# Kernel optimization log

Hardware: AMD Instinct MI355X
Metric: run time of the kernel (lower is better)

Reference implementation:

```python
import jax, jax.numpy as jnp
import numpy as np

B, S, D = 8, 2048, 1024      # batch, seq (tokens), in/out token dim
E = 2 * D                    # expansion dim (expansion_factor=2)
SDIM = 128                   # attention feature dim s
SQRT_S = float(np.sqrt(SDIM))
EPS_LN = 1e-5                # ScaleNorm eps


def setup_inputs() -> dict:
    key = jax.random.key(0)
    ks = jax.random.split(key, 8)
    return {
        "x": jax.random.normal(ks[0], (B, S, D), jnp.float32),
        "pos_enc": jax.random.normal(ks[1], (S, SDIM), jnp.float32),
        "ln_g": jnp.ones((1,), jnp.float32),                                   # ScaleNorm scalar gain
        "uv_w": jax.random.normal(ks[2], (2 * E + SDIM, D), jnp.float32) / np.sqrt(D),  # fused uv proj (xavier-ish)
        "gamma": jax.random.uniform(ks[3], (2, SDIM), jnp.float32),            # q/k affine scale
        "beta": jax.random.uniform(ks[4], (2, SDIM), jnp.float32),             # q/k affine shift
        "o_w": jax.random.normal(ks[5], (D, E), jnp.float32) / np.sqrt(E),     # output proj
        "res_scale": jnp.ones((D,), jnp.float32),                              # ChannelWiseScale
    }


def reference(x, pos_enc, ln_g, uv_w, gamma, beta, o_w, res_scale):
    # ScaleNorm: x / clamp(||x|| * d^-0.5, eps) * g
    norm = jnp.linalg.norm(x, axis=-1, keepdims=True) * (D ** -0.5)
    xn = x / jnp.maximum(norm, EPS_LN) * ln_g
    # fused uv projection + SiLU
    uv = jax.nn.silu(xn @ uv_w.T)                      # [B,S,2E+s]
    u = uv[..., :E]                                    # gate
    v = uv[..., E:2 * E]                               # values
    base = uv[..., 2 * E:]                             # shared q/k base [B,S,s]
    qk_base = base[..., None, :] * gamma + beta        # [B,S,2,s]
    q = qk_base[..., 0, :] + pos_enc                   # add positional enc [B,S,s]
    k = qk_base[..., 1, :] + pos_enc
    # squared-ReLU attention kernel
    kernel = jnp.square(jax.nn.relu(jnp.einsum('bqs,bks->bqk', q, k) / SQRT_S))
    out = (u * jnp.einsum('bqk,bke->bqe', kernel, v)) @ o_w.T  # [B,S,D]
    # channel-wise scaled residual (in_dims == out_dims -> shortcut)
    return x * res_scale + out
```

## Files before the change

### kernel.cpp

```cpp
#include <hip/hip_runtime.h>
#include <stdint.h>

#define B_   8
#define S_   2048
#define D_   1024
#define E_   2048
#define SD_  128
#define M_   (B_ * S_)
#define NUV  (2 * E_ + SD_)

typedef __attribute__((ext_vector_type(8))) short short8;
typedef __attribute__((ext_vector_type(4))) float floatx4;

__device__ __forceinline__ ushort f2bf(float f) {
    uint32_t u = __float_as_uint(f);
    uint32_t r = (u + 0x7fffu + ((u >> 16) & 1u)) >> 16;
    return (ushort)r;
}
__device__ __forceinline__ float bf2f(ushort h) {
    return __uint_as_float(((uint32_t)h) << 16);
}
__device__ __forceinline__ float silu(float z) {
    return z * __builtin_amdgcn_rcpf(1.0f + __expf(-z));
}

__device__ __forceinline__ void tile_swizzle(int& mt, int& nt) {
    const int gx  = gridDim.x;
    const int lin = blockIdx.y * gx + blockIdx.x;
    const int band = lin / (gx * 8);
    const int r    = lin - band * gx * 8;
    mt = band * 8 + (r & 7);
    nt = r >> 3;
}

__device__ __forceinline__ void gemm_core(
    const ushort* __restrict__ A, const ushort* __restrict__ B,
    int lda, int ldb, int K, int m0, int n0,
    ushort* ldsA, ushort* ldsB, floatx4 acc[4][4])
{
    const int t    = threadIdx.x;
    const int lane = t & 63;
    const int l15  = lane & 15;
    const int quad = lane >> 4;
    const int wave = t >> 6;
    const int wm   = (wave >> 1) * 64;
    const int wn   = (wave & 1) * 64;
    const int key  = l15 & 7;

    const ushort* gA[4]; const ushort* gB[4];
    ushort* lA[4]; ushort* lB[4];
    #pragma unroll
    for (int i = 0; i < 4; ++i) {
        const int c   = t + i * 256;
        const int row = c >> 3;
        const int gkc = ((c & 7) ^ (row & 7)) * 8;
        gA[i] = A + (size_t)(m0 + row) * lda + gkc;
        gB[i] = B + (size_t)(n0 + row) * ldb + gkc;
        lA[i] = ldsA + c * 8;
        lB[i] = ldsB + c * 8;
    }

    short8 rA[4], rB[4];
    #pragma unroll
    for (int i = 0; i < 4; ++i) rA[i] = *(const short8*)gA[i];
    #pragma unroll
    for (int i = 0; i < 4; ++i) rB[i] = *(const short8*)gB[i];

    for (int kk = 0; kk < K; kk += 64) {
        __syncthreads();
        #pragma unroll
        for (int i = 0; i < 4; ++i) *(short8*)lA[i] = rA[i];
        #pragma unroll
        for (int i = 0; i < 4; ++i) *(short8*)lB[i] = rB[i];
        __syncthreads();

        if (kk + 64 < K) {
            #pragma unroll
            for (int i = 0; i < 4; ++i) rA[i] = *(const short8*)(gA[i] + kk + 64);
            #pragma unroll
            for (int i = 0; i < 4; ++i) rB[i] = *(const short8*)(gB[i] + kk + 64);
        }

        #pragma unroll
        for (int s = 0; s < 2; ++s) {
            const int koff = ((s * 4 + quad) ^ key) * 8;
            short8 af[4], bfr[4];
            #pragma unroll
            for (int mi = 0; mi < 4; ++mi)
                af[mi] = *(const short8*)(ldsA + (wm + mi * 16 + l15) * 64 + koff);
            #pragma unroll
            for (int ni = 0; ni < 4; ++ni)
                bfr[ni] = *(const short8*)(ldsB + (wn + ni * 16 + l15) * 64 + koff);
            #pragma unroll
            for (int mi = 0; mi < 4; ++mi)
                #pragma unroll
                for (int ni = 0; ni < 4; ++ni)
                    acc[mi][ni] = __builtin_amdgcn_mfma_f32_16x16x32_bf16(
                        af[mi], bfr[ni], acc[mi][ni], 0, 0, 0);
        }
    }
}

#define EPI_INDICES \
    const int t = threadIdx.x; \
    const int lane = t & 63, l15 = lane & 15, quad = lane >> 4; \
    const int wave = t >> 6, wm = (wave >> 1) * 64, wn = (wave & 1) * 64; \
    (void)t;

#define ZERO_ACC \
    floatx4 acc[4][4]; \
    _Pragma("unroll") \
    for (int i = 0; i < 4; ++i) \
        _Pragma("unroll") \
        for (int j = 0; j < 4; ++j) \
            _Pragma("unroll") \
            for (int r = 0; r < 4; ++r) acc[i][j][r] = 0.0f;

__global__ __launch_bounds__(256) void k_cvt(const float* __restrict__ src,
                                             ushort* __restrict__ dst, int n4) {
    int i = blockIdx.x * 256 + threadIdx.x;
    if (i < n4) {
        float4 v = ((const float4*)src)[i];
        ushort4 o;
        o.x = f2bf(v.x); o.y = f2bf(v.y); o.z = f2bf(v.z); o.w = f2bf(v.w);
        ((ushort4*)dst)[i] = o;
    }
}

__global__ __launch_bounds__(256) void k_rmsnorm(const float* __restrict__ x,
                                                 const float* __restrict__ ln_g,
                                                 ushort* __restrict__ xnb) {
    const int m = blockIdx.x;
    const int t = threadIdx.x;
    float4 v = ((const float4*)(x + (size_t)m * D_))[t];
    float ss = v.x * v.x + v.y * v.y + v.z * v.z + v.w * v.w;
    #pragma unroll
    for (int off = 32; off > 0; off >>= 1) ss += __shfl_down(ss, off, 64);
    __shared__ float red[4];
    if ((t & 63) == 0) red[t >> 6] = ss;
    __syncthreads();
    float tot = red[0] + red[1] + red[2] + red[3];
    float rms = sqrtf(tot * (1.0f / (float)D_));
    float scale = ln_g[0] / fmaxf(rms, 1e-5f);
    ushort4 o;
    o.x = f2bf(v.x * scale); o.y = f2bf(v.y * scale);
    o.z = f2bf(v.z * scale); o.w = f2bf(v.w * scale);
    ((ushort4*)(xnb + (size_t)m * D_))[t] = o;
}

__global__ __launch_bounds__(256) void k_gemm1(
    const ushort* __restrict__ xnb, const ushort* __restrict__ uvwb,
    const float* __restrict__ gamma, const float* __restrict__ beta,
    const float* __restrict__ pos,
    ushort* __restrict__ u, ushort* __restrict__ vT,
    ushort* __restrict__ qb, ushort* __restrict__ kb)
{
    __shared__ __align__(16) ushort lds[17408];
    ushort* ldsA = lds;
    ushort* ldsB = lds + 8192;
    ZERO_ACC
    int mt, nt;
    tile_swizzle(mt, nt);
    const int m0 = mt * 128;
    const int n0 = nt * 128;
    gemm_core(xnb, uvwb, D_, D_, D_, m0, n0, ldsA, ldsB, acc);
    EPI_INDICES

    if (nt < 16) {
        #pragma unroll
        for (int mi = 0; mi < 4; ++mi)
            #pragma unroll
            for (int ni = 0; ni < 4; ++ni) {
                const int col = n0 + wn + ni * 16 + l15;
                #pragma unroll
                for (int r = 0; r < 4; ++r) {
                    const int row = m0 + wm + mi * 16 + quad * 4 + r;
                    u[(size_t)row * E_ + col] = f2bf(silu(acc[mi][ni][r]));
                }
            }
    } else if (nt < 32) {
        const int b   = m0 >> 11;
        const int s0  = m0 & (S_ - 1);
        const int ec0 = n0 - E_;
        __syncthreads();
        #pragma unroll
        for (int mi = 0; mi < 4; ++mi)
            #pragma unroll
            for (int ni = 0; ni < 4; ++ni) {
                const int col = wn + ni * 16 + l15;
                const int row = wm + mi * 16 + quad * 4;
                #pragma unroll
                for (int r = 0; r < 4; r += 2) {
                    ushort2 pr;
                    pr.x = f2bf(silu(acc[mi][ni][r]));
                    pr.y = f2bf(silu(acc[mi][ni][r + 1]));
                    *(ushort2*)&lds[col * 136 + row + r] = pr;
                }
            }
        __syncthreads();
        ushort* vTb = vT + ((size_t)b * E_ + ec0) * S_ + s0;
        #pragma unroll
        for (int i = 0; i < 8; ++i) {
            const int lin = i * 256 + t;
            const int e  = lin >> 4;
            const int sb = (lin & 15) * 8;
            *(short8*)(vTb + (size_t)e * S_ + sb) = *(const short8*)&lds[e * 136 + sb];
        }
    } else {
        #pragma unroll
        for (int mi = 0; mi < 4; ++mi)
            #pragma unroll
            for (int ni = 0; ni < 4; ++ni) {
                const int sd = wn + ni * 16 + l15;
                const float g0 = gamma[sd], g1 = gamma[SD_ + sd];
                const float be0 = beta[sd], be1 = beta[SD_ + sd];
                #pragma unroll
                for (int r = 0; r < 4; ++r) {
                    const int row = m0 + wm + mi * 16 + quad * 4 + r;
                    const int srow = row & (S_ - 1);
                    float s = silu(acc[mi][ni][r]);
                    const float p = pos[(size_t)srow * SD_ + sd];
                    qb[(size_t)row * SD_ + sd] = f2bf(s * g0 + be0 + p);
                    kb[(size_t)row * SD_ + sd] = f2bf(s * g1 + be1 + p);
                }
            }
    }
}

__global__ __launch_bounds__(256) void k_scores(
    const ushort* __restrict__ qb, const ushort* __restrict__ kb,
    ushort* __restrict__ kern, int b_off)
{
    __shared__ __align__(16) ushort ldsA[128 * 64];
    __shared__ __align__(16) ushort ldsB[128 * 64];
    ZERO_ACC
    const int bz = blockIdx.z;
    const int b  = b_off + bz;
    int mt, nt;
    tile_swizzle(mt, nt);
    const int m0 = mt * 128;
    const int n0 = nt * 128;
    gemm_core(qb + (size_t)b * S_ * SD_, kb + (size_t)b * S_ * SD_,
              SD_, SD_, SD_, m0, n0, ldsA, ldsB, acc);
    EPI_INDICES
    ushort* ko = kern + (size_t)bz * S_ * S_;
    const float inv = 0.08838834764831845f;
    #pragma unroll
    for (int mi = 0; mi < 4; ++mi)
        #pragma unroll
        for (int ni = 0; ni < 4; ++ni) {
            const int col = n0 + wn + ni * 16 + l15;
            #pragma unroll
            for (int r = 0; r < 4; ++r) {
                const int row = m0 + wm + mi * 16 + quad * 4 + r;
                float s = fmaxf(acc[mi][ni][r] * inv, 0.0f);
                ko[(size_t)row * S_ + col] = f2bf(s * s);
            }
        }
}

__global__ __launch_bounds__(256) void k_kv(
    const ushort* __restrict__ kern, const ushort* __restrict__ vT,
    const ushort* __restrict__ u, ushort* __restrict__ kvu, int b_off)
{
    __shared__ __align__(16) ushort ldsA[128 * 64];
    __shared__ __align__(16) ushort ldsB[128 * 64];
    ZERO_ACC
    const int bz = blockIdx.z;
    const int b  = b_off + bz;
    int mt, nt;
    tile_swizzle(mt, nt);
    const int m0 = mt * 128;
    const int n0 = nt * 128;
    gemm_core(kern + (size_t)bz * S_ * S_, vT + (size_t)b * E_ * S_,
              S_, S_, S_, m0, n0, ldsA, ldsB, acc);
    EPI_INDICES
    #pragma unroll
    for (int mi = 0; mi < 4; ++mi)
        #pragma unroll
        for (int ni = 0; ni < 4; ++ni) {
            const int col = n0 + wn + ni * 16 + l15;
            #pragma unroll
            for (int r = 0; r < 4; ++r) {
                const int row = m0 + wm + mi * 16 + quad * 4 + r;
                const size_t gi = (size_t)(b * S_ + row) * E_ + col;
                float uval = bf2f(u[gi]);
                kvu[gi] = f2bf(uval * acc[mi][ni][r]);
            }
        }
}

__global__ __launch_bounds__(256) void k_out(
    const ushort* __restrict__ kvu, const ushort* __restrict__ owb,
    const float* __restrict__ x, const float* __restrict__ res_scale,
    float* __restrict__ out)
{
    __shared__ __align__(16) ushort ldsA[128 * 64];
    __shared__ __align__(16) ushort ldsB[128 * 64];
    ZERO_ACC
    int mt, nt;
    tile_swizzle(mt, nt);
    const int m0 = mt * 128;
    const int n0 = nt * 128;
    gemm_core(kvu, owb, E_, E_, E_, m0, n0, ldsA, ldsB, acc);
    EPI_INDICES
    #pragma unroll
    for (int mi = 0; mi < 4; ++mi)
        #pragma unroll
        for (int ni = 0; ni < 4; ++ni) {
            const int col = n0 + wn + ni * 16 + l15;
            const float rs = res_scale[col];
            #pragma unroll
            for (int r = 0; r < 4; ++r) {
                const int row = m0 + wm + mi * 16 + quad * 4 + r;
                const size_t gi = (size_t)row * D_ + col;
                out[gi] = x[gi] * rs + acc[mi][ni][r];
            }
        }
}

extern "C" void kernel_launch(void* const* d_in, const int* in_sizes, int n_in,
                              void* d_out, int out_size, void* d_ws, size_t ws_size,
                              hipStream_t stream)
{
    const float* x         = (const float*)d_in[0];
    const float* pos       = (const float*)d_in[1];
    const float* ln_g      = (const float*)d_in[2];
    const float* uv_w      = (const float*)d_in[3];
    const float* gamma     = (const float*)d_in[4];
    const float* beta      = (const float*)d_in[5];
    const float* o_w       = (const float*)d_in[6];
    const float* res_scale = (const float*)d_in[7];
    float* out = (float*)d_out;

    char* p = (char*)d_ws;
    ushort* region0 = (ushort*)p; p += (size_t)M_ * D_ * 2;
    ushort* uvwb    = (ushort*)p; p += (size_t)NUV * D_ * 2;
    ushort* owb     = (ushort*)p; p += (size_t)D_ * E_ * 2;
    ushort* u       = (ushort*)p; p += (size_t)M_ * E_ * 2;
    ushort* kvu     = (ushort*)p; p += (size_t)M_ * E_ * 2;
    ushort* vT      = (ushort*)p; p += (size_t)M_ * E_ * 2;
    ushort* qb      = (ushort*)p; p += (size_t)M_ * SD_ * 2;
    ushort* kb      = (ushort*)p; p += (size_t)M_ * SD_ * 2;

    ushort* xnb  = region0;
    ushort* kern = region0;

    k_cvt<<<(NUV * D_ / 4 + 255) / 256, 256, 0, stream>>>(uv_w, uvwb, NUV * D_ / 4);
    k_cvt<<<(D_ * E_ / 4 + 255) / 256, 256, 0, stream>>>(o_w, owb, D_ * E_ / 4);
    k_rmsnorm<<<M_, 256, 0, stream>>>(x, ln_g, xnb);
    k_gemm1<<<dim3(NUV / 128, M_ / 128), 256, 0, stream>>>(xnb, uvwb, gamma, beta, pos, u, vT, qb, kb);
    for (int g = 0; g < 2; ++g) {
        k_scores<<<dim3(S_ / 128, S_ / 128, 4), 256, 0, stream>>>(qb, kb, kern, g * 4);
        k_kv<<<dim3(E_ / 128, S_ / 128, 4), 256, 0, stream>>>(kern, vT, u, kvu, g * 4);
    }
    k_out<<<dim3(D_ / 128, M_ / 128), 256, 0, stream>>>(kvu, owb, x, res_scale, out);
}
```

Baseline: 648.5 us.

## Use direct global-to-LDS loads, finer tile swizzle, and raise occupancy bound

Replaces the register-staged global-to-LDS copy with global_load_lds DMA loads directly into shared memory. This drops the register prefetch, which frees VGPRs, and adds a min-blocks-per-CU of 3 to launch bounds on all GEMM kernels so more workgroups can be resident. Tile swizzle now groups N tiles in chunks of 4 within each 8-row band to improve L2 reuse. The cost is losing the software prefetch overlap: the loads are now issued and waited on between the two barriers, with no double buffering, so each K step may stall on memory latency.

```diff
diff --git a/kernel.cpp b/kernel.cpp
--- a/kernel.cpp
+++ b/kernel.cpp
@@ -12,6 +12,9 @@
 typedef __attribute__((ext_vector_type(8))) short short8;
 typedef __attribute__((ext_vector_type(4))) float floatx4;
 
+typedef __attribute__((address_space(1))) void as1_void;
+typedef __attribute__((address_space(3))) void as3_void;
+
 __device__ __forceinline__ ushort f2bf(float f) {
     uint32_t u = __float_as_uint(f);
     uint32_t r = (u + 0x7fffu + ((u >> 16) & 1u)) >> 16;
@@ -24,13 +27,27 @@
     return z * __builtin_amdgcn_rcpf(1.0f + __expf(-z));
 }
 
+__device__ __forceinline__ void gld_lds16(const ushort* g, ushort* l) {
+    __builtin_amdgcn_global_load_lds((const as1_void*)g, (as3_void*)l, 16, 0, 0);
+}
+
 __device__ __forceinline__ void tile_swizzle(int& mt, int& nt) {
     const int gx  = gridDim.x;
     const int lin = blockIdx.y * gx + blockIdx.x;
-    const int band = lin / (gx * 8);
-    const int r    = lin - band * gx * 8;
-    mt = band * 8 + (r & 7);
-    nt = r >> 3;
+    const int bandSz = gx * 8;
+    const int band = lin / bandSz;
+    const int rem  = lin - band * bandSz;
+    const int full = gx >> 2;
+    const int sc   = rem >> 5;
+    if (sc < full) {
+        const int r2 = rem & 31;
+        mt = band * 8 + (r2 & 7);
+        nt = sc * 4 + (r2 >> 3);
+    } else {
+        const int r3 = rem - full * 32;
+        mt = band * 8 + (r3 & 7);
+        nt = full * 4 + (r3 >> 3);
+    }
 }
 
 __device__ __forceinline__ void gemm_core(
@@ -60,26 +77,13 @@
         lB[i] = ldsB + c * 8;
     }
 
-    short8 rA[4], rB[4];
-    #pragma unroll
-    for (int i = 0; i < 4; ++i) rA[i] = *(const short8*)gA[i];
-    #pragma unroll
-    for (int i = 0; i < 4; ++i) rB[i] = *(const short8*)gB[i];
-
     for (int kk = 0; kk < K; kk += 64) {
         __syncthreads();
         #pragma unroll
-        for (int i = 0; i < 4; ++i) *(short8*)lA[i] = rA[i];
-        #pragma unroll
-        for (int i = 0; i < 4; ++i) *(short8*)lB[i] = rB[i];
+        for (int i = 0; i < 4; ++i) gld_lds16(gA[i] + kk, lA[i]);
+        #pragma unroll
+        for (int i = 0; i < 4; ++i) gld_lds16(gB[i] + kk, lB[i]);
         __syncthreads();
-
-        if (kk + 64 < K) {
-            #pragma unroll
-            for (int i = 0; i < 4; ++i) rA[i] = *(const short8*)(gA[i] + kk + 64);
-            #pragma unroll
-            for (int i = 0; i < 4; ++i) rB[i] = *(const short8*)(gB[i] + kk + 64);
-        }
 
         #pragma unroll
         for (int s = 0; s < 2; ++s) {
@@ -148,7 +152,7 @@
     ((ushort4*)(xnb + (size_t)m * D_))[t] = o;
 }
 
-__global__ __launch_bounds__(256) void k_gemm1(
+__global__ __launch_bounds__(256, 3) void k_gemm1(
     const ushort* __restrict__ xnb, const ushort* __restrict__ uvwb,
     const float* __restrict__ gamma, const float* __restrict__ beta,
     const float* __restrict__ pos,
@@ -227,7 +231,7 @@
     }
 }
 
-__global__ __launch_bounds__(256) void k_scores(
+__global__ __launch_bounds__(256, 3) void k_scores(
     const ushort* __restrict__ qb, const ushort* __restrict__ kb,
     ushort* __restrict__ kern, int b_off)
 {
@@ -259,7 +263,7 @@
         }
 }
 
-__global__ __launch_bounds__(256) void k_kv(
+__global__ __launch_bounds__(256, 3) void k_kv(
     const ushort* __restrict__ kern, const ushort* __restrict__ vT,
     const ushort* __restrict__ u, ushort* __restrict__ kvu, int b_off)
 {
@@ -290,7 +294,7 @@
         }
 }
 
-__global__ __launch_bounds__(256) void k_out(
+__global__ __launch_bounds__(256, 3) void k_out(
     const ushort* __restrict__ kvu, const ushort* __restrict__ owb,
     const float* __restrict__ x, const float* __restrict__ res_scale,
     float* __restrict__ out)
```

New measurement: 580.0 us. 10.6% less time.
